# Optimization experiments

Hardware: AMD Instinct MI355X
Metric: run time of the kernel (lower is better)

## Reference

```python
import jax, jax.numpy as jnp
import numpy as np

D_MODEL = 1024
NUM_HEADS = 16
D_K = D_MODEL // NUM_HEADS
SCALE = 1.0 / np.sqrt(D_K).astype(np.float32)
NEG_INF = -1.0e9


def setup_inputs() -> dict:
    key = jax.random.key(0)
    ks = jax.random.split(key, 9)
    B, S = 4, 2048
    query = jax.random.normal(ks[0], (B, S, D_MODEL), dtype=jnp.float32)
    key_t = jax.random.normal(ks[1], (B, S, D_MODEL), dtype=jnp.float32)
    value = jax.random.normal(ks[2], (B, S, D_MODEL), dtype=jnp.float32)
    mask = jax.random.randint(ks[3], (B, S), 0, 2, dtype=jnp.int32)
    init = 1.0 / np.sqrt(D_MODEL).astype(np.float32)
    W_q = jax.random.uniform(ks[4], (D_MODEL, D_MODEL), jnp.float32, -init, init)
    W_k = jax.random.uniform(ks[5], (D_MODEL, D_MODEL), jnp.float32, -init, init)
    W_v = jax.random.uniform(ks[6], (D_MODEL, D_MODEL), jnp.float32, -init, init)
    W_o = jax.random.uniform(ks[7], (D_MODEL, D_MODEL), jnp.float32, -init, init)
    b_o = jax.random.uniform(ks[8], (D_MODEL,), jnp.float32, -init, init)
    return {"query": query, "key": key_t, "value": value, "mask": mask,
            "W_q": W_q, "W_k": W_k, "W_v": W_v, "W_o": W_o, "b_o": b_o}


def reference(query, key, value, mask, W_q, W_k, W_v, W_o, b_o):
    B, S, _ = query.shape
    # projections -> [B, H, S, d_k]  (torch Linear: x @ W.T)
    def split_heads(x, W):
        y = jnp.einsum('bsd,ed->bse', x, W)
        return y.reshape(B, S, NUM_HEADS, D_K).transpose(0, 2, 1, 3)
    Q = split_heads(query, W_q)
    K = split_heads(key, W_k)
    V = split_heads(value, W_v)
    # scores [B, H, S, S]
    scores = jnp.einsum('bhqd,bhkd->bhqk', Q, K) * SCALE
    key_mask = (mask[:, None, None, :] != 0)  # [B,1,1,S] over key axis
    scores = jnp.where(key_mask, scores, NEG_INF)
    probs = jax.nn.softmax(scores, axis=-1)
    # dropout is identity (p=0 / eval mode)
    context = jnp.einsum('bhqk,bhkd->bhqd', probs, V)
    context = context.transpose(0, 2, 1, 3).reshape(B, S, D_MODEL)
    output = jnp.einsum('bsd,ed->bse', context, W_o) + b_o
    return output, probs.mean(axis=1)
```

## Files before the change

kernel.cpp:

```cpp
#include <hip/hip_runtime.h>

typedef unsigned short u16t;
typedef __bf16 bf16x8 __attribute__((ext_vector_type(8)));
typedef float f32x4 __attribute__((ext_vector_type(4)));

#define NB 4
#define NS 2048
#define ND 1024
#define NH 16
#define NDK 64
#define NEGINF -1.0e9f
#define SCALE2 0.18033688011112042f

#define LAB 40

__device__ __forceinline__ float fexp2(float x) { return __builtin_amdgcn_exp2f(x); }

__device__ __forceinline__ u16t f2bf(float f) {
  return __builtin_bit_cast(u16t, (__bf16)f);
}

#define ROR16(x, n) __builtin_bit_cast(float, __builtin_amdgcn_update_dpp(     \
    __builtin_bit_cast(int, (x)), __builtin_bit_cast(int, (x)),                \
    0x120 + (n), 0xF, 0xF, false))

__device__ __forceinline__ int swz(int row, int col) {
  return row * 64 + (col ^ ((row & 7) << 3));
}

template<typename TA> struct Stg;
template<> struct Stg<float> {
  f32x4 lo, hi;
  __device__ __forceinline__ void ld(const float* p) {
    lo = *(const f32x4*)p; hi = *(const f32x4*)(p + 4);
  }
  __device__ __forceinline__ bf16x8 get() const {
    bf16x8 r;
    r[0] = (__bf16)lo[0]; r[1] = (__bf16)lo[1]; r[2] = (__bf16)lo[2]; r[3] = (__bf16)lo[3];
    r[4] = (__bf16)hi[0]; r[5] = (__bf16)hi[1]; r[6] = (__bf16)hi[2]; r[7] = (__bf16)hi[3];
    return r;
  }
};
template<> struct Stg<u16t> {
  bf16x8 v;
  __device__ __forceinline__ void ld(const u16t* p) { v = *(const bf16x8*)p; }
  __device__ __forceinline__ bf16x8 get() const { return v; }
};

template<typename TA, int MODE>
__global__ __launch_bounds__(256, 2)
void gemm_nt(const TA* __restrict__ A, const float* __restrict__ Bm,
             void* __restrict__ Cv, const float* __restrict__ bias)
{
  const int K = 1024;
  __shared__ __attribute__((aligned(16))) u16t At[128 * LAB];
  __shared__ __attribute__((aligned(16))) u16t Bt[128 * LAB];

  const int tid  = threadIdx.x;
  const int w    = tid >> 6;
  const int lane = tid & 63;
  const int quad = lane >> 4;
  const int l16  = lane & 15;
  const int wm   = w >> 1, wn = w & 1;
  const int m0   = blockIdx.x * 128;
  const int n0   = blockIdx.y * 128;

  const f32x4 fz = {0.f, 0.f, 0.f, 0.f};
  f32x4 acc[4][4];
#pragma unroll
  for (int i = 0; i < 4; i++)
#pragma unroll
    for (int j = 0; j < 4; j++) acc[i][j] = fz;

  const int r0 = tid >> 2, cg = (tid & 3) * 8;
  const int r1 = r0 + 64;

  Stg<TA> sa0, sa1; Stg<float> sb0, sb1;
  sa0.ld(A  + (long)(m0 + r0) * K + cg);
  sa1.ld(A  + (long)(m0 + r1) * K + cg);
  sb0.ld(Bm + (long)(n0 + r0) * K + cg);
  sb1.ld(Bm + (long)(n0 + r1) * K + cg);

  for (int k0 = 0; k0 < K; k0 += 32) {
    __syncthreads();
    *(bf16x8*)&At[r0 * LAB + cg] = sa0.get();
    *(bf16x8*)&At[r1 * LAB + cg] = sa1.get();
    *(bf16x8*)&Bt[r0 * LAB + cg] = sb0.get();
    *(bf16x8*)&Bt[r1 * LAB + cg] = sb1.get();
    __syncthreads();
    if (k0 + 32 < K) {
      sa0.ld(A  + (long)(m0 + r0) * K + k0 + 32 + cg);
      sa1.ld(A  + (long)(m0 + r1) * K + k0 + 32 + cg);
      sb0.ld(Bm + (long)(n0 + r0) * K + k0 + 32 + cg);
      sb1.ld(Bm + (long)(n0 + r1) * K + k0 + 32 + cg);
    }

    bf16x8 af[4], bfv[4];
#pragma unroll
    for (int i = 0; i < 4; i++)
      af[i] = *(const bf16x8*)&At[(wm * 64 + i * 16 + l16) * LAB + quad * 8];
#pragma unroll
    for (int j = 0; j < 4; j++)
      bfv[j] = *(const bf16x8*)&Bt[(wn * 64 + j * 16 + l16) * LAB + quad * 8];
#pragma unroll
    for (int i = 0; i < 4; i++)
#pragma unroll
      for (int j = 0; j < 4; j++)
        acc[i][j] = __builtin_amdgcn_mfma_f32_16x16x32_bf16(af[i], bfv[j], acc[i][j], 0, 0, 0);
  }

#pragma unroll
  for (int i = 0; i < 4; i++) {
    const int rbase = m0 + wm * 64 + i * 16 + quad * 4;
#pragma unroll
    for (int j = 0; j < 4; j++) {
      const int col = n0 + wn * 64 + j * 16 + l16;
      float bv = 0.f;
      if (MODE == 0) bv = bias[col];
#pragma unroll
      for (int r = 0; r < 4; r++) {
        const int row = rbase + r;
        float v = acc[i][j][r];
        if (MODE == 0) {
          ((float*)Cv)[(long)row * ND + col] = v + bv;
        } else if (MODE == 1) {
          int b = row >> 11, s = row & 2047, h = col >> 6, d = col & 63;
          ((u16t*)Cv)[(((long)(b * NH + h)) * NS + s) * NDK + d] = f2bf(v);
        } else {
          int b = row >> 11, s = row & 2047, h = col >> 6, d = col & 63;
          ((u16t*)Cv)[(((long)(b * NH + h)) * NDK + d) * NS + s] = f2bf(v);
        }
      }
    }
  }
}

__global__ __launch_bounds__(512, 4)
void flash_ctx(const u16t* __restrict__ Qw, const u16t* __restrict__ Kw,
               const u16t* __restrict__ VTw, const int* __restrict__ mask,
               u16t* __restrict__ ctx, float* __restrict__ mo, float* __restrict__ lo)
{
  __shared__ __attribute__((aligned(16))) u16t Kt[64 * 64];
  __shared__ __attribute__((aligned(16))) u16t Vt[64 * 64];
  __shared__ __attribute__((aligned(16))) u16t Pt[8 * 16 * 64];
  __shared__ float biasl[NS];

  const int tid  = threadIdx.x;
  const int w    = tid >> 6;
  const int lane = tid & 63;
  const int quad = lane >> 4;
  const int l16  = lane & 15;
  const int bh   = blockIdx.y;
  const int b    = bh >> 4;
  const int h    = bh & 15;
  const int qw   = blockIdx.x * 128 + w * 16;
  const int pbase = w * 1024;

  for (int i = tid; i < NS; i += 512)
    biasl[i] = mask[b * NS + i] ? 0.f : NEGINF;

  bf16x8 qf[2];
#pragma unroll
  for (int kk = 0; kk < 2; kk++)
    qf[kk] = *(const bf16x8*)(Qw + ((long)bh * NS + qw + l16) * NDK + kk * 32 + quad * 8);

  const f32x4 fz = {0.f, 0.f, 0.f, 0.f};
  const f32x4 fm = {NEGINF, NEGINF, NEGINF, NEGINF};
  f32x4 cacc[4];
#pragma unroll
  for (int d = 0; d < 4; d++) cacc[d] = fz;
  f32x4 mrun = fm;
  f32x4 lrun = fz;

  const int kr0 = tid >> 3, kc0 = (tid & 7) * 8;
  const long kbase = (long)bh * NS;
  const long vbase = (long)bh * NDK;

  bf16x8 kv = *(const bf16x8*)(Kw  + (kbase + kr0) * NDK + kc0);
  bf16x8 vv = *(const bf16x8*)(VTw + (vbase + kr0) * NS + kc0);

  for (int kb = 0; kb < NS; kb += 64) {
    __syncthreads();
    *(bf16x8*)&Kt[swz(kr0, kc0)] = kv;
    *(bf16x8*)&Vt[swz(kr0, kc0)] = vv;
    __syncthreads();
    if (kb + 64 < NS) {
      kv = *(const bf16x8*)(Kw  + (kbase + kb + 64 + kr0) * NDK + kc0);
      vv = *(const bf16x8*)(VTw + (vbase + kr0) * NS + kb + 64 + kc0);
    }

    f32x4 s[4];
#pragma unroll
    for (int c = 0; c < 4; c++) {
      f32x4 a = fz;
#pragma unroll
      for (int kk = 0; kk < 2; kk++) {
        bf16x8 kf = *(const bf16x8*)&Kt[swz(c * 16 + l16, kk * 32 + quad * 8)];
        a = __builtin_amdgcn_mfma_f32_16x16x32_bf16(qf[kk], kf, a, 0, 0, 0);
      }
      s[c] = a;
    }

#pragma unroll
    for (int c = 0; c < 4; c++) {
      const float bias_c = biasl[kb + c * 16 + l16];
#pragma unroll
      for (int r = 0; r < 4; r++)
        s[c][r] = s[c][r] * SCALE2 + bias_c;
    }

    f32x4 mx = s[0];
#pragma unroll
    for (int c = 1; c < 4; c++)
#pragma unroll
      for (int r = 0; r < 4; r++) mx[r] = fmaxf(mx[r], s[c][r]);
#pragma unroll
    for (int r = 0; r < 4; r++) {
      float x = mx[r];
      x = fmaxf(x, ROR16(x, 1));
      x = fmaxf(x, ROR16(x, 2));
      x = fmaxf(x, ROR16(x, 4));
      x = fmaxf(x, ROR16(x, 8));
      mx[r] = x;
    }

    f32x4 alpha;
#pragma unroll
    for (int r = 0; r < 4; r++) {
      float mnew = fmaxf(mrun[r], mx[r]);
      alpha[r] = fexp2(mrun[r] - mnew);
      mrun[r] = mnew;
    }
#pragma unroll
    for (int c = 0; c < 4; c++)
#pragma unroll
      for (int r = 0; r < 4; r++) s[c][r] = fexp2(s[c][r] - mrun[r]);

    f32x4 sm = fz;
#pragma unroll
    for (int c = 0; c < 4; c++)
#pragma unroll
      for (int r = 0; r < 4; r++) sm[r] += s[c][r];
#pragma unroll
    for (int r = 0; r < 4; r++) {
      float x = sm[r];
      x += ROR16(x, 1);
      x += ROR16(x, 2);
      x += ROR16(x, 4);
      x += ROR16(x, 8);
      sm[r] = x;
    }
#pragma unroll
    for (int r = 0; r < 4; r++) lrun[r] = lrun[r] * alpha[r] + sm[r];
#pragma unroll
    for (int d = 0; d < 4; d++)
#pragma unroll
      for (int r = 0; r < 4; r++) cacc[d][r] *= alpha[r];

#pragma unroll
    for (int c = 0; c < 4; c++)
#pragma unroll
      for (int r = 0; r < 4; r++)
        Pt[pbase + swz(quad * 4 + r, c * 16 + l16)] = f2bf(s[c][r]);

#pragma unroll
    for (int d = 0; d < 4; d++)
#pragma unroll
      for (int kk = 0; kk < 2; kk++) {
        bf16x8 pf = *(const bf16x8*)&Pt[pbase + swz(l16, kk * 32 + quad * 8)];
        bf16x8 vf = *(const bf16x8*)&Vt[swz(d * 16 + l16, kk * 32 + quad * 8)];
        cacc[d] = __builtin_amdgcn_mfma_f32_16x16x32_bf16(pf, vf, cacc[d], 0, 0, 0);
      }
  }

  {
    f32x4 rinv;
#pragma unroll
    for (int r = 0; r < 4; r++) rinv[r] = 1.f / lrun[r];
#pragma unroll
    for (int d = 0; d < 4; d++)
#pragma unroll
      for (int r = 0; r < 4; r++) {
        int qg = qw + quad * 4 + r;
        int e  = h * NDK + d * 16 + l16;
        ctx[((long)(b * NS + qg)) * ND + e] = f2bf(cacc[d][r] * rinv[r]);
      }
    if (l16 == 0) {
#pragma unroll
      for (int r = 0; r < 4; r++) {
        int qg = qw + quad * 4 + r;
        mo[(long)bh * NS + qg] = mrun[r];
        lo[(long)bh * NS + qg] = lrun[r];
      }
    }
  }
}

__global__ __launch_bounds__(256, 3)
void probs_mean(const u16t* __restrict__ Qw, const u16t* __restrict__ Kw,
                const int* __restrict__ mask, const float* __restrict__ mo,
                const float* __restrict__ lo, float* __restrict__ outp)
{
  __shared__ __attribute__((aligned(16))) u16t Qt[128 * 64];
  __shared__ __attribute__((aligned(16))) u16t Kt2[128 * 64];
  __shared__ float ml[NH * 128];
  __shared__ float li[NH * 128];
  __shared__ float biasl[128];

  const int tid  = threadIdx.x;
  const int w    = tid >> 6;
  const int lane = tid & 63;
  const int quad = lane >> 4;
  const int l16  = lane & 15;
  const int wm   = w >> 1, wn = w & 1;
  const int b  = blockIdx.z;
  const int q0 = blockIdx.y * 128;
  const int k0 = blockIdx.x * 128;

  for (int i = tid; i < NH * 128; i += 256) {
    int hh = i >> 7, r = i & 127;
    ml[i] = mo[((long)(b * NH + hh)) * NS + q0 + r];
    li[i] = 1.f / lo[((long)(b * NH + hh)) * NS + q0 + r];
  }
  for (int i = tid; i < 128; i += 256)
    biasl[i] = mask[b * NS + k0 + i] ? 0.f : NEGINF;

  const f32x4 fz = {0.f, 0.f, 0.f, 0.f};
  f32x4 acc[4][4];
#pragma unroll
  for (int i = 0; i < 4; i++)
#pragma unroll
    for (int j = 0; j < 4; j++) acc[i][j] = fz;

  bf16x8 qv[4], kv[4];
#pragma unroll
  for (int rr = 0; rr < 4; rr++) {
    int idx = rr * 256 + tid;
    int row = idx >> 3, off = (idx & 7) * 8;
    qv[rr] = *(const bf16x8*)(Qw + ((long)(b * NH) * NS + q0 + row) * NDK + off);
    kv[rr] = *(const bf16x8*)(Kw + ((long)(b * NH) * NS + k0 + row) * NDK + off);
  }

  for (int hh = 0; hh < NH; hh++) {
    __syncthreads();
#pragma unroll
    for (int rr = 0; rr < 4; rr++) {
      int idx = rr * 256 + tid;
      int row = idx >> 3, off = (idx & 7) * 8;
      *(bf16x8*)&Qt[swz(row, off)]  = qv[rr];
      *(bf16x8*)&Kt2[swz(row, off)] = kv[rr];
    }
    __syncthreads();
    if (hh + 1 < NH) {
#pragma unroll
      for (int rr = 0; rr < 4; rr++) {
        int idx = rr * 256 + tid;
        int row = idx >> 3, off = (idx & 7) * 8;
        qv[rr] = *(const bf16x8*)(Qw + ((long)(b * NH + hh + 1) * NS + q0 + row) * NDK + off);
        kv[rr] = *(const bf16x8*)(Kw + ((long)(b * NH + hh + 1) * NS + k0 + row) * NDK + off);
      }
    }

    bf16x8 af[4][2], bfv[4][2];
#pragma unroll
    for (int i = 0; i < 4; i++)
#pragma unroll
      for (int kk = 0; kk < 2; kk++) {
        af[i][kk]  = *(const bf16x8*)&Qt[swz(wm * 64 + i * 16 + l16, kk * 32 + quad * 8)];
        bfv[i][kk] = *(const bf16x8*)&Kt2[swz(wn * 64 + i * 16 + l16, kk * 32 + quad * 8)];
      }
#pragma unroll
    for (int i = 0; i < 4; i++)
#pragma unroll
      for (int j = 0; j < 4; j++) {
        f32x4 s = fz;
#pragma unroll
        for (int kk = 0; kk < 2; kk++)
          s = __builtin_amdgcn_mfma_f32_16x16x32_bf16(af[i][kk], bfv[j][kk], s, 0, 0, 0);
        const float bias_c = biasl[wn * 64 + j * 16 + l16];
#pragma unroll
        for (int r = 0; r < 4; r++) {
          int rowb = wm * 64 + i * 16 + quad * 4 + r;
          float p = fexp2(s[r] * SCALE2 + bias_c - ml[hh * 128 + rowb]) * li[hh * 128 + rowb];
          acc[i][j][r] += p;
        }
      }
  }

#pragma unroll
  for (int i = 0; i < 4; i++)
#pragma unroll
    for (int j = 0; j < 4; j++)
#pragma unroll
      for (int r = 0; r < 4; r++) {
        int row = q0 + wm * 64 + i * 16 + quad * 4 + r;
        int col = k0 + wn * 64 + j * 16 + l16;
        outp[((long)(b * NS + row)) * NS + col] = acc[i][j][r] * (1.f / 16.f);
      }
}

extern "C" void kernel_launch(void* const* d_in, const int* in_sizes, int n_in,
                              void* d_out, int out_size, void* d_ws, size_t ws_size,
                              hipStream_t stream)
{
  (void)in_sizes; (void)n_in; (void)out_size; (void)ws_size;
  const float* query = (const float*)d_in[0];
  const float* keyt  = (const float*)d_in[1];
  const float* value = (const float*)d_in[2];
  const int*   mask  = (const int*)d_in[3];
  const float* Wq = (const float*)d_in[4];
  const float* Wk = (const float*)d_in[5];
  const float* Wv = (const float*)d_in[6];
  const float* Wo = (const float*)d_in[7];
  const float* bo = (const float*)d_in[8];

  float* out  = (float*)d_out;
  float* outp = out + (long)NB * NS * ND;

  u16t* q_ws  = (u16t*)d_ws;
  u16t* k_ws  = q_ws + (long)NB * NH * NS * NDK;
  u16t* vt_ws = k_ws + (long)NB * NH * NS * NDK;
  float* m_ws = (float*)(vt_ws + (long)NB * NH * NS * NDK);
  float* l_ws = m_ws + (long)NB * NH * NS;
  u16t* ctx_ws = (u16t*)outp;

  dim3 blk(256);
  gemm_nt<float, 1><<<dim3(64, 8), blk, 0, stream>>>(query, Wq, q_ws, nullptr);
  gemm_nt<float, 1><<<dim3(64, 8), blk, 0, stream>>>(keyt,  Wk, k_ws, nullptr);
  gemm_nt<float, 2><<<dim3(64, 8), blk, 0, stream>>>(value, Wv, vt_ws, nullptr);
  flash_ctx<<<dim3(NS / 128, NB * NH), dim3(512), 0, stream>>>(q_ws, k_ws, vt_ws, mask,
                                                               ctx_ws, m_ws, l_ws);
  gemm_nt<u16t, 0><<<dim3(64, 8), blk, 0, stream>>>(ctx_ws, Wo, out, bo);
  probs_mean<<<dim3(NS / 128, NS / 128, NB), blk, 0, stream>>>(q_ws, k_ws, mask,
                                                               m_ws, l_ws, outp);
}
```

Baseline: 518.3 us.

## Batch QKV projections into one launch, hoist P fragments, stream softmax stats

Merges the three Q/K/V projection GEMMs into a single launch with a z-grid dimension, so 1536 blocks fill the GPU at once instead of three smaller grids with tails. In flash_ctx the P fragment loads are taken out of the d loop, so each is read from LDS once instead of four times. In probs_mean the per-head max and 1/l values are now prefetched one head ahead into small LDS buffers instead of preloading all 16 heads up front. The last change cuts LDS use, which may raise occupancy, but adds a per-head reciprocal and per-head global loads.

```diff
diff --git a/kernel.cpp b/kernel.cpp
--- a/kernel.cpp
+++ b/kernel.cpp
@@ -47,14 +47,21 @@
   __device__ __forceinline__ bf16x8 get() const { return v; }
 };
 
-template<typename TA, int MODE>
 __global__ __launch_bounds__(256, 2)
-void gemm_nt(const TA* __restrict__ A, const float* __restrict__ Bm,
-             void* __restrict__ Cv, const float* __restrict__ bias)
+void qkv_proj(const float* __restrict__ Aq, const float* __restrict__ Ak,
+              const float* __restrict__ Av,
+              const float* __restrict__ Wq, const float* __restrict__ Wk,
+              const float* __restrict__ Wv,
+              u16t* __restrict__ Cq, u16t* __restrict__ Ck, u16t* __restrict__ Cvp)
 {
   const int K = 1024;
   __shared__ __attribute__((aligned(16))) u16t At[128 * LAB];
   __shared__ __attribute__((aligned(16))) u16t Bt[128 * LAB];
+
+  const int z = blockIdx.z;
+  const float* A  = (z == 0) ? Aq : (z == 1) ? Ak : Av;
+  const float* Bm = (z == 0) ? Wq : (z == 1) ? Wk : Wv;
+  u16t* C = (z == 0) ? Cq : (z == 1) ? Ck : Cvp;
 
   const int tid  = threadIdx.x;
   const int w    = tid >> 6;
@@ -75,7 +82,7 @@
   const int r0 = tid >> 2, cg = (tid & 3) * 8;
   const int r1 = r0 + 64;
 
-  Stg<TA> sa0, sa1; Stg<float> sb0, sb1;
+  Stg<float> sa0, sa1, sb0, sb1;
   sa0.ld(A  + (long)(m0 + r0) * K + cg);
   sa1.ld(A  + (long)(m0 + r1) * K + cg);
   sb0.ld(Bm + (long)(n0 + r0) * K + cg);
@@ -115,22 +122,90 @@
 #pragma unroll
     for (int j = 0; j < 4; j++) {
       const int col = n0 + wn * 64 + j * 16 + l16;
-      float bv = 0.f;
-      if (MODE == 0) bv = bias[col];
 #pragma unroll
       for (int r = 0; r < 4; r++) {
         const int row = rbase + r;
-        float v = acc[i][j][r];
-        if (MODE == 0) {
-          ((float*)Cv)[(long)row * ND + col] = v + bv;
-        } else if (MODE == 1) {
-          int b = row >> 11, s = row & 2047, h = col >> 6, d = col & 63;
-          ((u16t*)Cv)[(((long)(b * NH + h)) * NS + s) * NDK + d] = f2bf(v);
-        } else {
-          int b = row >> 11, s = row & 2047, h = col >> 6, d = col & 63;
-          ((u16t*)Cv)[(((long)(b * NH + h)) * NDK + d) * NS + s] = f2bf(v);
-        }
-      }
+        int b = row >> 11, s = row & 2047, h = col >> 6, d = col & 63;
+        if (z < 2)
+          C[(((long)(b * NH + h)) * NS + s) * NDK + d] = f2bf(acc[i][j][r]);
+        else
+          C[(((long)(b * NH + h)) * NDK + d) * NS + s] = f2bf(acc[i][j][r]);
+      }
+    }
+  }
+}
+
+__global__ __launch_bounds__(256, 2)
+void gemm_out(const u16t* __restrict__ A, const float* __restrict__ Bm,
+              float* __restrict__ Cv, const float* __restrict__ bias)
+{
+  const int K = 1024;
+  __shared__ __attribute__((aligned(16))) u16t At[128 * LAB];
+  __shared__ __attribute__((aligned(16))) u16t Bt[128 * LAB];
+
+  const int tid  = threadIdx.x;
+  const int w    = tid >> 6;
+  const int lane = tid & 63;
+  const int quad = lane >> 4;
+  const int l16  = lane & 15;
+  const int wm   = w >> 1, wn = w & 1;
+  const int m0   = blockIdx.x * 128;
+  const int n0   = blockIdx.y * 128;
+
+  const f32x4 fz = {0.f, 0.f, 0.f, 0.f};
+  f32x4 acc[4][4];
+#pragma unroll
+  for (int i = 0; i < 4; i++)
+#pragma unroll
+    for (int j = 0; j < 4; j++) acc[i][j] = fz;
+
+  const int r0 = tid >> 2, cg = (tid & 3) * 8;
+  const int r1 = r0 + 64;
+
+  Stg<u16t> sa0, sa1; Stg<float> sb0, sb1;
+  sa0.ld(A  + (long)(m0 + r0) * K + cg);
+  sa1.ld(A  + (long)(m0 + r1) * K + cg);
+  sb0.ld(Bm + (long)(n0 + r0) * K + cg);
+  sb1.ld(Bm + (long)(n0 + r1) * K + cg);
+
+  for (int k0 = 0; k0 < K; k0 += 32) {
+    __syncthreads();
+    *(bf16x8*)&At[r0 * LAB + cg] = sa0.get();
+    *(bf16x8*)&At[r1 * LAB + cg] = sa1.get();
+    *(bf16x8*)&Bt[r0 * LAB + cg] = sb0.get();
+    *(bf16x8*)&Bt[r1 * LAB + cg] = sb1.get();
+    __syncthreads();
+    if (k0 + 32 < K) {
+      sa0.ld(A  + (long)(m0 + r0) * K + k0 + 32 + cg);
+      sa1.ld(A  + (long)(m0 + r1) * K + k0 + 32 + cg);
+      sb0.ld(Bm + (long)(n0 + r0) * K + k0 + 32 + cg);
+      sb1.ld(Bm + (long)(n0 + r1) * K + k0 + 32 + cg);
+    }
+
+    bf16x8 af[4], bfv[4];
+#pragma unroll
+    for (int i = 0; i < 4; i++)
+      af[i] = *(const bf16x8*)&At[(wm * 64 + i * 16 + l16) * LAB + quad * 8];
+#pragma unroll
+    for (int j = 0; j < 4; j++)
+      bfv[j] = *(const bf16x8*)&Bt[(wn * 64 + j * 16 + l16) * LAB + quad * 8];
+#pragma unroll
+    for (int i = 0; i < 4; i++)
+#pragma unroll
+      for (int j = 0; j < 4; j++)
+        acc[i][j] = __builtin_amdgcn_mfma_f32_16x16x32_bf16(af[i], bfv[j], acc[i][j], 0, 0, 0);
+  }
+
+#pragma unroll
+  for (int i = 0; i < 4; i++) {
+    const int rbase = m0 + wm * 64 + i * 16 + quad * 4;
+#pragma unroll
+    for (int j = 0; j < 4; j++) {
+      const int col = n0 + wn * 64 + j * 16 + l16;
+      const float bv = bias[col];
+#pragma unroll
+      for (int r = 0; r < 4; r++)
+        Cv[(long)(rbase + r) * ND + col] = acc[i][j][r] + bv;
     }
   }
 }
@@ -263,13 +338,16 @@
       for (int r = 0; r < 4; r++)
         Pt[pbase + swz(quad * 4 + r, c * 16 + l16)] = f2bf(s[c][r]);
 
+    bf16x8 pf[2];
+#pragma unroll
+    for (int kk = 0; kk < 2; kk++)
+      pf[kk] = *(const bf16x8*)&Pt[pbase + swz(l16, kk * 32 + quad * 8)];
 #pragma unroll
     for (int d = 0; d < 4; d++)
 #pragma unroll
       for (int kk = 0; kk < 2; kk++) {
-        bf16x8 pf = *(const bf16x8*)&Pt[pbase + swz(l16, kk * 32 + quad * 8)];
         bf16x8 vf = *(const bf16x8*)&Vt[swz(d * 16 + l16, kk * 32 + quad * 8)];
-        cacc[d] = __builtin_amdgcn_mfma_f32_16x16x32_bf16(pf, vf, cacc[d], 0, 0, 0);
+        cacc[d] = __builtin_amdgcn_mfma_f32_16x16x32_bf16(pf[kk], vf, cacc[d], 0, 0, 0);
       }
   }
 
@@ -303,8 +381,8 @@
 {
   __shared__ __attribute__((aligned(16))) u16t Qt[128 * 64];
   __shared__ __attribute__((aligned(16))) u16t Kt2[128 * 64];
-  __shared__ float ml[NH * 128];
-  __shared__ float li[NH * 128];
+  __shared__ float mlc[128];
+  __shared__ float lic[128];
   __shared__ float biasl[128];
 
   const int tid  = threadIdx.x;
@@ -317,11 +395,6 @@
   const int q0 = blockIdx.y * 128;
   const int k0 = blockIdx.x * 128;
 
-  for (int i = tid; i < NH * 128; i += 256) {
-    int hh = i >> 7, r = i & 127;
-    ml[i] = mo[((long)(b * NH + hh)) * NS + q0 + r];
-    li[i] = 1.f / lo[((long)(b * NH + hh)) * NS + q0 + r];
-  }
   for (int i = tid; i < 128; i += 256)
     biasl[i] = mask[b * NS + k0 + i] ? 0.f : NEGINF;
 
@@ -340,6 +413,8 @@
     qv[rr] = *(const bf16x8*)(Qw + ((long)(b * NH) * NS + q0 + row) * NDK + off);
     kv[rr] = *(const bf16x8*)(Kw + ((long)(b * NH) * NS + k0 + row) * NDK + off);
   }
+  float mlpref = (tid < 128) ? mo[((long)(b * NH)) * NS + q0 + tid]
+                             : lo[((long)(b * NH)) * NS + q0 + (tid & 127)];
 
   for (int hh = 0; hh < NH; hh++) {
     __syncthreads();
@@ -350,6 +425,8 @@
       *(bf16x8*)&Qt[swz(row, off)]  = qv[rr];
       *(bf16x8*)&Kt2[swz(row, off)] = kv[rr];
     }
+    if (tid < 128) mlc[tid] = mlpref;
+    else           lic[tid & 127] = 1.f / mlpref;
     __syncthreads();
     if (hh + 1 < NH) {
 #pragma unroll
@@ -359,6 +436,8 @@
         qv[rr] = *(const bf16x8*)(Qw + ((long)(b * NH + hh + 1) * NS + q0 + row) * NDK + off);
         kv[rr] = *(const bf16x8*)(Kw + ((long)(b * NH + hh + 1) * NS + k0 + row) * NDK + off);
       }
+      mlpref = (tid < 128) ? mo[((long)(b * NH + hh + 1)) * NS + q0 + tid]
+                           : lo[((long)(b * NH + hh + 1)) * NS + q0 + (tid & 127)];
     }
 
     bf16x8 af[4][2], bfv[4][2];
@@ -381,7 +460,7 @@
 #pragma unroll
         for (int r = 0; r < 4; r++) {
           int rowb = wm * 64 + i * 16 + quad * 4 + r;
-          float p = fexp2(s[r] * SCALE2 + bias_c - ml[hh * 128 + rowb]) * li[hh * 128 + rowb];
+          float p = fexp2(s[r] * SCALE2 + bias_c - mlc[rowb]) * lic[rowb];
           acc[i][j][r] += p;
         }
       }
@@ -425,12 +504,11 @@
   u16t* ctx_ws = (u16t*)outp;
 
   dim3 blk(256);
-  gemm_nt<float, 1><<<dim3(64, 8), blk, 0, stream>>>(query, Wq, q_ws, nullptr);
-  gemm_nt<float, 1><<<dim3(64, 8), blk, 0, stream>>>(keyt,  Wk, k_ws, nullptr);
-  gemm_nt<float, 2><<<dim3(64, 8), blk, 0, stream>>>(value, Wv, vt_ws, nullptr);
+  qkv_proj<<<dim3(64, 8, 3), blk, 0, stream>>>(query, keyt, value, Wq, Wk, Wv,
+                                               q_ws, k_ws, vt_ws);
   flash_ctx<<<dim3(NS / 128, NB * NH), dim3(512), 0, stream>>>(q_ws, k_ws, vt_ws, mask,
                                                                ctx_ws, m_ws, l_ws);
-  gemm_nt<u16t, 0><<<dim3(64, 8), blk, 0, stream>>>(ctx_ws, Wo, out, bo);
+  gemm_out<<<dim3(64, 8), blk, 0, stream>>>(ctx_ws, Wo, out, bo);
   probs_mean<<<dim3(NS / 128, NS / 128, NB), blk, 0, stream>>>(q_ws, k_ws, mask,
                                                                m_ws, l_ws, outp);
 }
```

After: 543.0 us. +4.8%, slower.
